# Kernel tuning notes

Measured on AMD Instinct MI355X. Metric: run time of the kernel, lower is better.

The kernel has to match this reference:

```python
import jax, jax.numpy as jnp
import numpy as np

N_NODES = 100000
N_EDGES = 3200000
N_FEAT = 256
N_HID = 64


def setup_inputs() -> dict:
    key = jax.random.key(0)
    k1, k2, k3, k4, k5 = jax.random.split(key, 5)
    edge_index = jax.random.randint(k1, (2, N_EDGES), 0, N_NODES, dtype=jnp.int64 if jax.config.jax_enable_x64 else jnp.int32)
    x = jax.random.normal(k2, (N_NODES, N_FEAT), dtype=jnp.float32)
    s_est = 1.0 / np.sqrt(N_FEAT)
    W_est = jax.random.uniform(k3, (N_FEAT, 1), jnp.float32, -s_est, s_est)
    b_est = jnp.zeros((1,), jnp.float32)
    W_gnn = jax.random.uniform(k4, (N_FEAT, N_HID), jnp.float32, -s_est, s_est)
    b_gnn = jnp.zeros((N_HID,), jnp.float32)
    s_cls = 1.0 / np.sqrt(N_HID)
    W_cls = jax.random.uniform(k5, (N_HID, 1), jnp.float32, -s_cls, s_cls)
    b_cls = jnp.zeros((1,), jnp.float32)
    return {"edge_index": edge_index, "x": x, "W_est": W_est, "b_est": b_est,
            "W_gnn": W_gnn, "b_gnn": b_gnn, "W_cls": W_cls, "b_cls": b_cls}


def _gcn_norm(edge_index, n):
    # PyG GCNConv default: add self-loops, symmetric normalization D^-1/2 (A+I) D^-1/2
    loops = jnp.arange(n, dtype=edge_index.dtype)
    row = jnp.concatenate([edge_index[0], loops])  # source
    col = jnp.concatenate([edge_index[1], loops])  # target
    deg = jax.ops.segment_sum(jnp.ones_like(col, dtype=jnp.float32), col, num_segments=n)
    dinv = jnp.where(deg > 0, jax.lax.rsqrt(jnp.maximum(deg, 1.0)), 0.0)
    norm = dinv[row] * dinv[col]  # [E+N]
    return row, col, norm


def _gcn_conv(x, W, b, row, col, norm, n):
    h = x @ W                              # [N, out] transform first (PyG order)
    msg = norm[:, None] * h[row]           # gather over sources, [E+N, out]
    out = jax.ops.segment_sum(msg, col, num_segments=n)  # scatter-add to targets
    return out + b


def reference(edge_index, x, W_est, b_est, W_gnn, b_gnn, W_cls, b_cls):
    n = x.shape[0]
    row, col, norm = _gcn_norm(edge_index, n)
    s = _gcn_conv(x, W_est, b_est, row, col, norm, n)   # estimator: GCNConv(nfeat, 1)
    z = _gcn_conv(x, W_gnn, b_gnn, row, col, norm, n)   # GNN: GCNConv(nfeat, 64)
    y = z @ W_cls + b_cls                                # classifier head
    return (y, s)
```

## Files before the change

### kernel.cpp

```cpp
#include <hip/hip_runtime.h>

#define N_NODES 100000
#define N_EDGES 3200000
#define N_FEAT  256
#define N_HID   64

#define NBINS     256
#define BIN_W     391
#define BIN_CAP   13568
#define NPART     500
#define EPB       6400
#define I4PB      1600
#define NPQ       25000

__global__ void k_wcomb(const float* __restrict__ Wg, const float* __restrict__ bg,
                        const float* __restrict__ Wc, const float* __restrict__ bc,
                        float* __restrict__ wcomb, float* __restrict__ biasy,
                        int* __restrict__ cursor) {
    int f = threadIdx.x;
    if (f < NBINS) cursor[f] = 0;
    float s = 0.f;
#pragma unroll
    for (int k = 0; k < N_HID; ++k) s += Wg[f * N_HID + k] * Wc[k];
    wcomb[f] = s;
    if (f == 0) {
        float b = 0.f;
        for (int k = 0; k < N_HID; ++k) b += bg[k] * Wc[k];
        *biasy = b + bc[0];
    }
}

__global__ __launch_bounds__(256) void k_pqpart(
        const float* __restrict__ x, const float* __restrict__ West,
        const float* __restrict__ wcomb, float2* __restrict__ pq,
        const int4* __restrict__ row4, const int4* __restrict__ col4,
        int* __restrict__ cursor, unsigned int* __restrict__ grouped) {
    __shared__ int cnts[256];
    __shared__ int lstart[256];
    __shared__ int lcount[256];
    __shared__ int gbase[256];
    __shared__ int scan[256];
    __shared__ unsigned int stage[EPB];

    int tid = threadIdx.x;

    if (blockIdx.x >= NPART) {
        int node = (((int)blockIdx.x - NPART) << 2) + (tid >> 6);
        int lane = tid & 63;
        if (node >= N_NODES) return;
        float4 v  = ((const float4*)(x + (size_t)node * N_FEAT))[lane];
        float4 we = ((const float4*)West)[lane];
        float4 wc = ((const float4*)wcomb)[lane];
        float ps = v.x * we.x + v.y * we.y + v.z * we.z + v.w * we.w;
        float qs = v.x * wc.x + v.y * wc.y + v.z * wc.z + v.w * wc.w;
#pragma unroll
        for (int off = 32; off > 0; off >>= 1) {
            ps += __shfl_down(ps, off);
            qs += __shfl_down(qs, off);
        }
        if (lane == 0) pq[node] = make_float2(qs, ps);
        return;
    }

    lcount[tid] = 0;
    __syncthreads();
    int i0 = blockIdx.x * I4PB;

    for (int i = i0 + tid; i < i0 + I4PB; i += 256) {
        int4 c = col4[i];
        atomicAdd(&lcount[c.x / BIN_W], 1);
        atomicAdd(&lcount[c.y / BIN_W], 1);
        atomicAdd(&lcount[c.z / BIN_W], 1);
        atomicAdd(&lcount[c.w / BIN_W], 1);
    }
    __syncthreads();

    int cnt = lcount[tid];
    cnts[tid] = cnt;
    scan[tid] = cnt;
    __syncthreads();
#pragma unroll
    for (int d = 1; d < 256; d <<= 1) {
        int t = (tid >= d) ? scan[tid - d] : 0;
        __syncthreads();
        scan[tid] += t;
        __syncthreads();
    }
    lstart[tid] = scan[tid] - cnt;
    gbase[tid]  = (cnt > 0) ? atomicAdd(&cursor[tid], cnt) : 0;
    lcount[tid] = 0;
    __syncthreads();

    for (int i = i0 + tid; i < i0 + I4PB; i += 256) {
        int4 c = col4[i];
        int4 r = row4[i];
        int b0 = c.x / BIN_W; int s0 = lstart[b0] + atomicAdd(&lcount[b0], 1);
        stage[s0] = ((unsigned)(c.x - b0 * BIN_W) << 17) | (unsigned)r.x;
        int b1 = c.y / BIN_W; int s1 = lstart[b1] + atomicAdd(&lcount[b1], 1);
        stage[s1] = ((unsigned)(c.y - b1 * BIN_W) << 17) | (unsigned)r.y;
        int b2 = c.z / BIN_W; int s2 = lstart[b2] + atomicAdd(&lcount[b2], 1);
        stage[s2] = ((unsigned)(c.z - b2 * BIN_W) << 17) | (unsigned)r.z;
        int b3 = c.w / BIN_W; int s3 = lstart[b3] + atomicAdd(&lcount[b3], 1);
        stage[s3] = ((unsigned)(c.w - b3 * BIN_W) << 17) | (unsigned)r.w;
    }
    __syncthreads();

    int wid = tid >> 6, lane = tid & 63;
    for (int b = wid; b < NBINS; b += 4) {
        int s = lstart[b], len = cnts[b], gb = gbase[b];
        unsigned int* dst = grouped + (size_t)b * BIN_CAP;
        for (int off = lane; off < len; off += 64) {
            int g = gb + off;
            if (g < BIN_CAP) dst[g] = stage[s + off];
        }
    }
}

__global__ __launch_bounds__(256) void k_bindeg(const int* __restrict__ cursor,
                                                const unsigned int* __restrict__ grouped,
                                                const float2* __restrict__ pq,
                                                float* __restrict__ dinv,
                                                float2* __restrict__ table) {
    __shared__ int dh[BIN_W];
    int b = blockIdx.x, tid = threadIdx.x;
    for (int i = tid; i < BIN_W; i += 256) dh[i] = 0;
    __syncthreads();
    int cnt = cursor[b];
    if (cnt > BIN_CAP) cnt = BIN_CAP;
    const unsigned int* g = grouped + (size_t)b * BIN_CAP;
    for (int i = tid; i < cnt; i += 256) atomicAdd(&dh[g[i] >> 17], 1);
    __syncthreads();
    for (int l = tid; l < BIN_W; l += 256) {
        int node = b * BIN_W + l;
        if (node < N_NODES) {
            float di = rsqrtf((float)(dh[l] + 1));
            dinv[node] = di;
            float2 v = pq[node];
            table[node] = make_float2(di * v.x, di * v.y);
        }
    }
}

__global__ __launch_bounds__(1024) void k_binacc(const int* __restrict__ cursor,
                                                 const unsigned int* __restrict__ grouped,
                                                 const float2* __restrict__ table,
                                                 const float* __restrict__ dinv,
                                                 const float* __restrict__ biasy,
                                                 const float* __restrict__ best,
                                                 float* __restrict__ out) {
    __shared__ float2 tile[BIN_W];
    int b = blockIdx.x, tid = threadIdx.x;
    for (int l = tid; l < BIN_W; l += 1024) {
        int node = b * BIN_W + l;
        tile[l] = (node < N_NODES) ? table[node] : make_float2(0.f, 0.f);
    }
    __syncthreads();
    int cnt = cursor[b];
    if (cnt > BIN_CAP) cnt = BIN_CAP;
    const unsigned int* g = grouped + (size_t)b * BIN_CAP;
    for (int i = tid; i < cnt; i += 1024) {
        unsigned int v = g[i];
        float2 t = table[v & 0x1FFFFu];
        int lc = v >> 17;
        atomicAdd(&tile[lc].x, t.x);
        atomicAdd(&tile[lc].y, t.y);
    }
    __syncthreads();
    float by = biasy[0], bs = best[0];
    for (int l = tid; l < BIN_W; l += 1024) {
        int node = b * BIN_W + l;
        if (node < N_NODES) {
            float di = dinv[node];
            out[node]           = di * tile[l].x + by;
            out[N_NODES + node] = di * tile[l].y + bs;
        }
    }
}

__global__ __launch_bounds__(256) void k_deg_fb(const int* __restrict__ col,
                                                int* __restrict__ deg) {
    int e = blockIdx.x * blockDim.x + threadIdx.x;
    if (e < N_EDGES) atomicAdd(&deg[col[e]], 1);
}
__global__ __launch_bounds__(256) void k_pqtable_fb(
        const float* __restrict__ x, const float* __restrict__ West,
        const float* __restrict__ wcomb, const int* __restrict__ deg,
        float* __restrict__ dinv, float2* __restrict__ table,
        float2* __restrict__ acc) {
    int node = (blockIdx.x * blockDim.x + threadIdx.x) >> 6;
    int lane = threadIdx.x & 63;
    if (node >= N_NODES) return;
    float4 v  = ((const float4*)(x + (size_t)node * N_FEAT))[lane];
    float4 we = ((const float4*)West)[lane];
    float4 wc = ((const float4*)wcomb)[lane];
    float ps = v.x * we.x + v.y * we.y + v.z * we.z + v.w * we.w;
    float qs = v.x * wc.x + v.y * wc.y + v.z * wc.z + v.w * wc.w;
#pragma unroll
    for (int off = 32; off > 0; off >>= 1) {
        ps += __shfl_down(ps, off);
        qs += __shfl_down(qs, off);
    }
    if (lane == 0) {
        float di = rsqrtf((float)(deg[node] + 1));
        float2 t = make_float2(di * qs, di * ps);
        dinv[node] = di; table[node] = t; acc[node] = t;
    }
}
__global__ __launch_bounds__(256) void k_edge_fb(const int* __restrict__ ei,
                                                 const float2* __restrict__ table,
                                                 float2* __restrict__ acc) {
    int e = blockIdx.x * blockDim.x + threadIdx.x;
    if (e >= N_EDGES) return;
    float2 t = table[ei[e]];
    int c = ei[N_EDGES + e];
    unsafeAtomicAdd(&acc[c].x, t.x);
    unsafeAtomicAdd(&acc[c].y, t.y);
}
__global__ __launch_bounds__(256) void k_fin_fb(
        const float* __restrict__ dinv, const float2* __restrict__ acc,
        const float* __restrict__ biasy, const float* __restrict__ best,
        float* __restrict__ out) {
    int i = blockIdx.x * blockDim.x + threadIdx.x;
    if (i >= N_NODES) return;
    float di = dinv[i];
    float2 a = acc[i];
    out[i]           = di * a.x + biasy[0];
    out[N_NODES + i] = di * a.y + best[0];
}

extern "C" void kernel_launch(void* const* d_in, const int* in_sizes, int n_in,
                              void* d_out, int out_size, void* d_ws, size_t ws_size,
                              hipStream_t stream) {
    const int*   ei   = (const int*)d_in[0];
    const float* x    = (const float*)d_in[1];
    const float* West = (const float*)d_in[2];
    const float* best = (const float*)d_in[3];
    const float* Wg   = (const float*)d_in[4];
    const float* bg   = (const float*)d_in[5];
    const float* Wc   = (const float*)d_in[6];
    const float* bc   = (const float*)d_in[7];
    float* out = (float*)d_out;

    char* ws = (char*)d_ws;
    float*  wcomb = (float*)ws;
    float*  biasy = wcomb + 256;
    float2* pq    = (float2*)(ws + 2048);
    float2* table = (float2*)(ws + 802048);
    float*  dinv  = (float*)(ws + 1602048);
    int*    cursor= (int*)(ws + 2002048);
    unsigned int* grouped = (unsigned int*)(ws + 2003072);
    size_t need = 2003072 + (size_t)NBINS * BIN_CAP * 4;

    if (ws_size >= need) {
        k_wcomb<<<1, 256, 0, stream>>>(Wg, bg, Wc, bc, wcomb, biasy, cursor);
        k_pqpart<<<NPART + NPQ, 256, 0, stream>>>(x, West, wcomb, pq,
                                                  (const int4*)ei,
                                                  (const int4*)(ei + N_EDGES),
                                                  cursor, grouped);
        k_bindeg<<<NBINS, 256, 0, stream>>>(cursor, grouped, pq, dinv, table);
        k_binacc<<<NBINS, 1024, 0, stream>>>(cursor, grouped, table, dinv,
                                             biasy, best, out);
    } else {
        int*    deg  = (int*)(ws + 2048 + 800000 * 2 + 400000);
        float2* acc  = pq;
        float2* tbl  = table;
        hipMemsetAsync(deg, 0, N_NODES * sizeof(int), stream);
        k_wcomb<<<1, 256, 0, stream>>>(Wg, bg, Wc, bc, wcomb, biasy, (int*)(ws + 2002048));
        k_deg_fb<<<(N_EDGES + 255) / 256, 256, 0, stream>>>(ei + N_EDGES, deg);
        k_pqtable_fb<<<(N_NODES * 64 + 255) / 256, 256, 0, stream>>>(
            x, West, wcomb, deg, dinv, tbl, acc);
        k_edge_fb<<<(N_EDGES + 255) / 256, 256, 0, stream>>>(ei, tbl, acc);
        k_fin_fb<<<(N_NODES + 255) / 256, 256, 0, stream>>>(dinv, acc, biasy, best, out);
    }
}
```

Measured before the change: 101.1 us.

## Replace atomic-cursor binning with histogram, scan, and deterministic scatter passes

Splits the fused partition kernel into separate pq, per-block histogram, single-block serial scan, and scatter kernels, so each block's global offset per bin comes from a prefix scan instead of global atomics on a cursor. Partition blocks are halved in size and doubled in count. The accumulate kernel now reads two grouped entries per thread and uses split x/y shared arrays. This adds three extra launches, a serial 1000-step scan, and a second pass over col, in exchange for removing global atomic contention and the mixed fused kernel.

Measured after the change: 161.4 us. 1.6x slower.

```diff
diff --git a/kernel.cpp b/kernel.cpp
--- a/kernel.cpp
+++ b/kernel.cpp
@@ -8,17 +8,14 @@
 #define NBINS     256
 #define BIN_W     391
 #define BIN_CAP   13568
-#define NPART     500
-#define EPB       6400
-#define I4PB      1600
-#define NPQ       25000
+#define NPART     1000
+#define EPB       3200
+#define I4PB      800
 
 __global__ void k_wcomb(const float* __restrict__ Wg, const float* __restrict__ bg,
                         const float* __restrict__ Wc, const float* __restrict__ bc,
-                        float* __restrict__ wcomb, float* __restrict__ biasy,
-                        int* __restrict__ cursor) {
+                        float* __restrict__ wcomb, float* __restrict__ biasy) {
     int f = threadIdx.x;
-    if (f < NBINS) cursor[f] = 0;
     float s = 0.f;
 #pragma unroll
     for (int k = 0; k < N_HID; ++k) s += Wg[f * N_HID + k] * Wc[k];
@@ -30,54 +27,74 @@
     }
 }
 
-__global__ __launch_bounds__(256) void k_pqpart(
-        const float* __restrict__ x, const float* __restrict__ West,
-        const float* __restrict__ wcomb, float2* __restrict__ pq,
-        const int4* __restrict__ row4, const int4* __restrict__ col4,
-        int* __restrict__ cursor, unsigned int* __restrict__ grouped) {
-    __shared__ int cnts[256];
-    __shared__ int lstart[256];
-    __shared__ int lcount[256];
-    __shared__ int gbase[256];
-    __shared__ int scan[256];
-    __shared__ unsigned int stage[EPB];
-
+__global__ __launch_bounds__(256) void k_pq(const float* __restrict__ x,
+                                            const float* __restrict__ West,
+                                            const float* __restrict__ wcomb,
+                                            float2* __restrict__ pq) {
+    int node = (blockIdx.x * blockDim.x + threadIdx.x) >> 6;
+    int lane = threadIdx.x & 63;
+    if (node >= N_NODES) return;
+    float4 v  = ((const float4*)(x + (size_t)node * N_FEAT))[lane];
+    float4 we = ((const float4*)West)[lane];
+    float4 wc = ((const float4*)wcomb)[lane];
+    float ps = v.x * we.x + v.y * we.y + v.z * we.z + v.w * we.w;
+    float qs = v.x * wc.x + v.y * wc.y + v.z * wc.z + v.w * wc.w;
+#pragma unroll
+    for (int off = 32; off > 0; off >>= 1) {
+        ps += __shfl_down(ps, off);
+        qs += __shfl_down(qs, off);
+    }
+    if (lane == 0) pq[node] = make_float2(qs, ps);
+}
+
+__global__ __launch_bounds__(256) void k_hist(const int4* __restrict__ col4,
+                                              int* __restrict__ hist) {
+    __shared__ int h[NBINS];
     int tid = threadIdx.x;
-
-    if (blockIdx.x >= NPART) {
-        int node = (((int)blockIdx.x - NPART) << 2) + (tid >> 6);
-        int lane = tid & 63;
-        if (node >= N_NODES) return;
-        float4 v  = ((const float4*)(x + (size_t)node * N_FEAT))[lane];
-        float4 we = ((const float4*)West)[lane];
-        float4 wc = ((const float4*)wcomb)[lane];
-        float ps = v.x * we.x + v.y * we.y + v.z * we.z + v.w * we.w;
-        float qs = v.x * wc.x + v.y * wc.y + v.z * wc.z + v.w * wc.w;
-#pragma unroll
-        for (int off = 32; off > 0; off >>= 1) {
-            ps += __shfl_down(ps, off);
-            qs += __shfl_down(qs, off);
-        }
-        if (lane == 0) pq[node] = make_float2(qs, ps);
-        return;
-    }
-
-    lcount[tid] = 0;
+    h[tid] = 0;
     __syncthreads();
     int i0 = blockIdx.x * I4PB;
-
     for (int i = i0 + tid; i < i0 + I4PB; i += 256) {
         int4 c = col4[i];
-        atomicAdd(&lcount[c.x / BIN_W], 1);
-        atomicAdd(&lcount[c.y / BIN_W], 1);
-        atomicAdd(&lcount[c.z / BIN_W], 1);
-        atomicAdd(&lcount[c.w / BIN_W], 1);
-    }
-    __syncthreads();
-
-    int cnt = lcount[tid];
-    cnts[tid] = cnt;
-    scan[tid] = cnt;
+        atomicAdd(&h[c.x / BIN_W], 1);
+        atomicAdd(&h[c.y / BIN_W], 1);
+        atomicAdd(&h[c.z / BIN_W], 1);
+        atomicAdd(&h[c.w / BIN_W], 1);
+    }
+    __syncthreads();
+    hist[blockIdx.x * NBINS + tid] = h[tid];
+}
+
+__global__ __launch_bounds__(256) void k_scan(const int* __restrict__ hist,
+                                              int* __restrict__ base,
+                                              int* __restrict__ cursor) {
+    int t = threadIdx.x;
+    int run = 0;
+    for (int blk = 0; blk < NPART; ++blk) {
+        int v = hist[blk * NBINS + t];
+        base[blk * NBINS + t] = run;
+        run += v;
+    }
+    cursor[t] = run;
+}
+
+__global__ __launch_bounds__(256) void k_scatter(const int4* __restrict__ row4,
+                                                 const int4* __restrict__ col4,
+                                                 const int* __restrict__ hist,
+                                                 const int* __restrict__ base,
+                                                 unsigned int* __restrict__ grouped) {
+    __shared__ int cnts[NBINS];
+    __shared__ int lstart[NBINS];
+    __shared__ int lcount[NBINS];
+    __shared__ int gbase[NBINS];
+    __shared__ int scan[NBINS];
+    __shared__ unsigned int stage[EPB];
+    int tid = threadIdx.x;
+    int cnt = hist[blockIdx.x * NBINS + tid];
+    cnts[tid]   = cnt;
+    gbase[tid]  = base[blockIdx.x * NBINS + tid];
+    scan[tid]   = cnt;
+    lcount[tid] = 0;
     __syncthreads();
 #pragma unroll
     for (int d = 1; d < 256; d <<= 1) {
@@ -87,10 +104,9 @@
         __syncthreads();
     }
     lstart[tid] = scan[tid] - cnt;
-    gbase[tid]  = (cnt > 0) ? atomicAdd(&cursor[tid], cnt) : 0;
-    lcount[tid] = 0;
-    __syncthreads();
-
+    __syncthreads();
+
+    int i0 = blockIdx.x * I4PB;
     for (int i = i0 + tid; i < i0 + I4PB; i += 256) {
         int4 c = col4[i];
         int4 r = row4[i];
@@ -108,11 +124,9 @@
     int wid = tid >> 6, lane = tid & 63;
     for (int b = wid; b < NBINS; b += 4) {
         int s = lstart[b], len = cnts[b], gb = gbase[b];
-        unsigned int* dst = grouped + (size_t)b * BIN_CAP;
-        for (int off = lane; off < len; off += 64) {
-            int g = gb + off;
-            if (g < BIN_CAP) dst[g] = stage[s + off];
-        }
+        unsigned int* dst = grouped + (size_t)b * BIN_CAP + gb;
+        for (int off = lane; off < len; off += 64)
+            if (gb + off < BIN_CAP) dst[off] = stage[s + off];
     }
 }
 
@@ -148,22 +162,36 @@
                                                  const float* __restrict__ biasy,
                                                  const float* __restrict__ best,
                                                  float* __restrict__ out) {
-    __shared__ float2 tile[BIN_W];
+    __shared__ float tx[BIN_W];
+    __shared__ float ty[BIN_W];
     int b = blockIdx.x, tid = threadIdx.x;
     for (int l = tid; l < BIN_W; l += 1024) {
         int node = b * BIN_W + l;
-        tile[l] = (node < N_NODES) ? table[node] : make_float2(0.f, 0.f);
+        float2 t = (node < N_NODES) ? table[node] : make_float2(0.f, 0.f);
+        tx[l] = t.x;
+        ty[l] = t.y;
     }
     __syncthreads();
     int cnt = cursor[b];
     if (cnt > BIN_CAP) cnt = BIN_CAP;
     const unsigned int* g = grouped + (size_t)b * BIN_CAP;
-    for (int i = tid; i < cnt; i += 1024) {
-        unsigned int v = g[i];
+    const uint2* g2 = (const uint2*)g;
+    int n2 = cnt >> 1;
+    for (int i = tid; i < n2; i += 1024) {
+        uint2 v = g2[i];
+        float2 ta = table[v.x & 0x1FFFFu];
+        float2 tb = table[v.y & 0x1FFFFu];
+        int la = v.x >> 17, lb = v.y >> 17;
+        atomicAdd(&tx[la], ta.x);
+        atomicAdd(&ty[la], ta.y);
+        atomicAdd(&tx[lb], tb.x);
+        atomicAdd(&ty[lb], tb.y);
+    }
+    if (tid == 0 && (cnt & 1)) {
+        unsigned int v = g[cnt - 1];
         float2 t = table[v & 0x1FFFFu];
-        int lc = v >> 17;
-        atomicAdd(&tile[lc].x, t.x);
-        atomicAdd(&tile[lc].y, t.y);
+        atomicAdd(&tx[v >> 17], t.x);
+        atomicAdd(&ty[v >> 17], t.y);
     }
     __syncthreads();
     float by = biasy[0], bs = best[0];
@@ -171,8 +199,8 @@
         int node = b * BIN_W + l;
         if (node < N_NODES) {
             float di = dinv[node];
-            out[node]           = di * tile[l].x + by;
-            out[N_NODES + node] = di * tile[l].y + bs;
+            out[node]           = di * tx[l] + by;
+            out[N_NODES + node] = di * ty[l] + bs;
         }
     }
 }
@@ -249,14 +277,18 @@
     float*  dinv  = (float*)(ws + 1602048);
     int*    cursor= (int*)(ws + 2002048);
     unsigned int* grouped = (unsigned int*)(ws + 2003072);
-    size_t need = 2003072 + (size_t)NBINS * BIN_CAP * 4;
+    int*    hist  = (int*)(ws + 2003072 + (size_t)NBINS * BIN_CAP * 4);
+    int*    base  = hist + (size_t)NPART * NBINS;
+    size_t need = 2003072 + (size_t)NBINS * BIN_CAP * 4 + (size_t)NPART * NBINS * 8;
 
     if (ws_size >= need) {
-        k_wcomb<<<1, 256, 0, stream>>>(Wg, bg, Wc, bc, wcomb, biasy, cursor);
-        k_pqpart<<<NPART + NPQ, 256, 0, stream>>>(x, West, wcomb, pq,
-                                                  (const int4*)ei,
-                                                  (const int4*)(ei + N_EDGES),
-                                                  cursor, grouped);
+        k_wcomb<<<1, 256, 0, stream>>>(Wg, bg, Wc, bc, wcomb, biasy);
+        k_pq<<<(N_NODES * 64 + 255) / 256, 256, 0, stream>>>(x, West, wcomb, pq);
+        k_hist<<<NPART, 256, 0, stream>>>((const int4*)(ei + N_EDGES), hist);
+        k_scan<<<1, 256, 0, stream>>>(hist, base, cursor);
+        k_scatter<<<NPART, 256, 0, stream>>>((const int4*)ei,
+                                             (const int4*)(ei + N_EDGES),
+                                             hist, base, grouped);
         k_bindeg<<<NBINS, 256, 0, stream>>>(cursor, grouped, pq, dinv, table);
         k_binacc<<<NBINS, 1024, 0, stream>>>(cursor, grouped, table, dinv,
                                              biasy, best, out);
@@ -265,7 +297,7 @@
         float2* acc  = pq;
         float2* tbl  = table;
         hipMemsetAsync(deg, 0, N_NODES * sizeof(int), stream);
-        k_wcomb<<<1, 256, 0, stream>>>(Wg, bg, Wc, bc, wcomb, biasy, (int*)(ws + 2002048));
+        k_wcomb<<<1, 256, 0, stream>>>(Wg, bg, Wc, bc, wcomb, biasy);
         k_deg_fb<<<(N_EDGES + 255) / 256, 256, 0, stream>>>(ei + N_EDGES, deg);
         k_pqtable_fb<<<(N_NODES * 64 + 255) / 256, 256, 0, stream>>>(
             x, West, wcomb, deg, dinv, tbl, acc);
```
